# Optimization experiments

Measured on AMD Instinct MI355X. Metric: run time of the kernel, lower is better.

Reference implementation:

```python
import jax, jax.numpy as jnp
import numpy as np
import itertools

B, N, C, D = 2, 150000, 64, 128  # samples, points/sample, channels, voxel grid extent
EPS = 1e-4  # BatchNormBlock eps
# 3x3x3 submanifold kernel offsets (27 taps)
OFFS = jnp.array(list(itertools.product((-1, 0, 1), repeat=3)), dtype=jnp.int32)  # [27,3]


def setup_inputs() -> dict:
    key = jax.random.key(0)
    k1, k2 = jax.random.split(key)
    rng = np.random.default_rng(0)
    # unique voxel coordinates per sample on a D^3 grid
    pos = np.stack([
        np.stack(np.unravel_index(rng.choice(D ** 3, size=N, replace=False), (D, D, D)), axis=-1)
        for _ in range(B)
    ]).astype(np.int32)  # [B,N,3]
    feats = jax.random.normal(k1, (B, N, C), jnp.float32)
    # 4 submanifold convs (2 residual blocks x 2 convs), fan-in scaled
    Ws = jax.random.normal(k2, (4, 27, C, C), jnp.float32) / np.sqrt(27 * C)
    gammas = jnp.ones((4, C), jnp.float32)
    betas = jnp.zeros((4, C), jnp.float32)
    return {"feats": feats, "Ws": Ws, "gammas": gammas, "betas": betas, "pos": jnp.asarray(pos)}


def _build_lut(pos_b):  # pos_b: [N,3] int32 -> dense hash grid [D^3] of point index or -1
    code = (pos_b[:, 0] * D + pos_b[:, 1]) * D + pos_b[:, 2]
    return jnp.full((D ** 3,), -1, jnp.int32).at[code].set(jnp.arange(N, dtype=jnp.int32))


def _subconv(x, lut_b, pos_b, W):
    # submanifold sparse conv: per kernel tap, gather neighbor features and GEMM
    # x:[N,C], lut_b:[D^3], pos_b:[N,3], W:[27,Cin,Cout]
    def step(acc, kw):
        d, Wk = kw
        npos = pos_b + d  # [N,3]
        valid = jnp.all((npos >= 0) & (npos < D), axis=-1)
        code = (npos[:, 0] * D + npos[:, 1]) * D + npos[:, 2]
        nidx = lut_b[jnp.where(valid, code, 0)]
        valid = valid & (nidx >= 0)
        g = jnp.where(valid[:, None], x[jnp.clip(nidx, 0, N - 1)], 0.0)  # [N,Cin]
        return acc + g @ Wk, None

    acc0 = jnp.zeros((x.shape[0], W.shape[-1]), x.dtype)
    acc, _ = jax.lax.scan(step, acc0, (OFFS, W))
    return acc


def _bn_relu(x, g, b):
    # BatchNormBlock (train mode, biased var over all concatenated points) + ReLU
    mu = x.mean(axis=(0, 1))
    var = jnp.mean(jnp.square(x - mu), axis=(0, 1))
    return jax.nn.relu((x - mu) * jax.lax.rsqrt(var + EPS) * g + b)


def reference(feats, Ws, gammas, betas, pos):
    lut = jax.vmap(_build_lut)(pos)  # [B, D^3]
    conv = jax.vmap(_subconv, in_axes=(0, 0, 0, None))
    x = feats
    for blk in range(2):  # conv_block_reps ResidualBlocks (NIN is Identity since nIn==nOut)
        out1 = x
        h = _bn_relu(x, gammas[2 * blk], betas[2 * blk])
        h = conv(h, lut, pos, Ws[2 * blk])
        h = _bn_relu(h, gammas[2 * blk + 1], betas[2 * blk + 1])
        out2 = conv(h, lut, pos, Ws[2 * blk + 1])
        x = out1 + out2
    return x
```

## Files before the change

### kernel.cpp

```cpp
#include <hip/hip_runtime.h>
#include <stdint.h>

#define DGRID 128
#define D3 (DGRID * DGRID * DGRID)
#define NBATCH 2
#define NPTS 150000
#define NROWS (NBATCH * NPTS)
#define NPAD 300032
#define NWAVES (NPAD / 64)
#define NCBLK (NWAVES / 4)
#define EPSBN 1e-4f
#define SBLK 1024

typedef __attribute__((ext_vector_type(8))) short s16x8;
typedef __attribute__((ext_vector_type(4))) float f32x4;

static __device__ __forceinline__ uint32_t f2bf_rne(float f) {
  uint32_t b = __float_as_uint(f);
  return (b + 0x7FFFu + ((b >> 16) & 1u)) >> 16;
}

static __device__ __forceinline__ f32x4 mfma16(uint4 a, uint4 b, f32x4 c) {
  return __builtin_amdgcn_mfma_f32_16x16x32_bf16(
      __builtin_bit_cast(s16x8, a), __builtin_bit_cast(s16x8, b), c, 0, 0, 0);
}

__global__ void k_scatter(const int* __restrict__ pos, int* __restrict__ lut) {
  int g = blockIdx.x * blockDim.x + threadIdx.x;
  if (g >= NROWS) return;
  int b = g / NPTS;
  int i = g - b * NPTS;
  int x = pos[3 * g], y = pos[3 * g + 1], z = pos[3 * g + 2];
  lut[(size_t)b * D3 + (x * DGRID + y) * DGRID + z] = i;
}

__global__ void k_nbr(const int* __restrict__ pos, const int* __restrict__ lut,
                      int* __restrict__ nbr) {
  int g = blockIdx.x * blockDim.x + threadIdx.x;
  if (g >= NROWS) return;
  int b = g / NPTS;
  int x = pos[3 * g], y = pos[3 * g + 1], z = pos[3 * g + 2];
  const int* L = lut + (size_t)b * D3;
#pragma unroll
  for (int t = 0; t < 27; ++t) {
    int nx = x + t / 9 - 1;
    int ny = y + (t / 3) % 3 - 1;
    int nz = z + t % 3 - 1;
    int v = -1;
    if ((unsigned)nx < DGRID && (unsigned)ny < DGRID && (unsigned)nz < DGRID) {
      int n = L[(nx * DGRID + ny) * DGRID + nz];
      if (n >= 0) v = b * NPTS + n;
    }
    nbr[(size_t)t * NPAD + g] = v;
  }
}

__global__ void k_wpack(const float* __restrict__ Ws, uint4* __restrict__ Wfrag) {
  int e = blockIdx.x * 256 + threadIdx.x;
  if (e >= 4 * 27 * 512) return;
  int lane = e & 63, nb = (e >> 6) & 3, s = (e >> 8) & 1, tt = e >> 9;
  int kb = s * 32 + (lane >> 4) * 8;
  int cout = nb * 16 + (lane & 15);
  const float* src = Ws + (size_t)tt * 4096;
  uint32_t p[4];
#pragma unroll
  for (int j = 0; j < 4; ++j) {
    uint32_t lo = f2bf_rne(src[(kb + 2 * j) * 64 + cout]);
    uint32_t hi = f2bf_rne(src[(kb + 2 * j + 1) * 64 + cout]);
    p[j] = (hi << 16) | lo;
  }
  uint4 o;
  o.x = p[0]; o.y = p[1]; o.z = p[2]; o.w = p[3];
  Wfrag[e] = o;
}

__global__ void k_stats1(const float* __restrict__ X, float* __restrict__ part) {
  __shared__ float s[512];
  int c = threadIdx.x & 63, q = threadIdx.x >> 6;
  float sm = 0.f, sq = 0.f;
  for (int r = blockIdx.x * 4 + q; r < NROWS; r += SBLK * 4) {
    float v = X[(size_t)r * 64 + c];
    sm += v;
    sq += v * v;
  }
  s[threadIdx.x] = sm;
  s[256 + threadIdx.x] = sq;
  __syncthreads();
  if (q == 0) {
    sm = s[c] + s[64 + c] + s[128 + c] + s[192 + c];
    sq = s[256 + c] + s[320 + c] + s[384 + c] + s[448 + c];
    part[blockIdx.x * 128 + c] = sm;
    part[blockIdx.x * 128 + 64 + c] = sq;
  }
}

__global__ void k_stats2(const float* __restrict__ part, int nblk,
                         const float* __restrict__ gamma, const float* __restrict__ beta,
                         float* __restrict__ chanp, int cid) {
  __shared__ float s[512];
  int c = threadIdx.x & 63, q = threadIdx.x >> 6;
  float sm = 0.f, sq = 0.f;
  for (int rb = q; rb < nblk; rb += 4) {
    sm += part[rb * 128 + c];
    sq += part[rb * 128 + 64 + c];
  }
  s[threadIdx.x] = sm;
  s[256 + threadIdx.x] = sq;
  __syncthreads();
  if (q == 0) {
    sm = s[c] + s[64 + c] + s[128 + c] + s[192 + c];
    sq = s[256 + c] + s[320 + c] + s[384 + c] + s[448 + c];
    float mean = sm / (float)NROWS;
    float var = sq / (float)NROWS - mean * mean;
    float a = gamma[cid * 64 + c] * rsqrtf(var + EPSBN);
    chanp[cid * 128 + c] = a;
    chanp[cid * 128 + 64 + c] = beta[cid * 64 + c] - mean * a;
  }
}

__global__ void k_hpass(const float* __restrict__ X, const float* __restrict__ chanp,
                        int cid, uint4* __restrict__ h) {
  int g = blockIdx.x * blockDim.x + threadIdx.x;
  if (g >= NROWS * 8) return;
  int c0 = (g & 7) * 8;
  const float* cp = chanp + cid * 128;
  const float4 a0 = *(const float4*)(cp + c0);
  const float4 a1 = *(const float4*)(cp + c0 + 4);
  const float4 b0 = *(const float4*)(cp + 64 + c0);
  const float4 b1 = *(const float4*)(cp + 64 + c0 + 4);
  const float4 x0 = *(const float4*)(X + (size_t)g * 8);
  const float4 x1 = *(const float4*)(X + (size_t)g * 8 + 4);
  float v0 = fmaxf(fmaf(x0.x, a0.x, b0.x), 0.f);
  float v1 = fmaxf(fmaf(x0.y, a0.y, b0.y), 0.f);
  float v2 = fmaxf(fmaf(x0.z, a0.z, b0.z), 0.f);
  float v3 = fmaxf(fmaf(x0.w, a0.w, b0.w), 0.f);
  float v4 = fmaxf(fmaf(x1.x, a1.x, b1.x), 0.f);
  float v5 = fmaxf(fmaf(x1.y, a1.y, b1.y), 0.f);
  float v6 = fmaxf(fmaf(x1.z, a1.z, b1.z), 0.f);
  float v7 = fmaxf(fmaf(x1.w, a1.w, b1.w), 0.f);
  uint4 o;
  o.x = (f2bf_rne(v1) << 16) | f2bf_rne(v0);
  o.y = (f2bf_rne(v3) << 16) | f2bf_rne(v2);
  o.z = (f2bf_rne(v5) << 16) | f2bf_rne(v4);
  o.w = (f2bf_rne(v7) << 16) | f2bf_rne(v6);
  h[g] = o;
}

__global__ __launch_bounds__(256, 4) void k_conv(
    const uint4* __restrict__ h, const uint4* __restrict__ Wf,
    const int* __restrict__ nbr, const float* __restrict__ res,
    float* __restrict__ out, float* __restrict__ part, int do_stats) {
  __shared__ uint4 wlds[2][512];
  __shared__ float sred[2][4][4][16];
  int tid = threadIdx.x;
  int wv = tid >> 6, lane = tid & 63;
  int tbase = (blockIdx.x * 4 + wv) * 64;
  int lrow = lane & 15, lkg = lane >> 4;

  f32x4 acc[4][4];
#pragma unroll
  for (int i = 0; i < 4; i++)
#pragma unroll
    for (int j = 0; j < 4; j++) acc[i][j] = (f32x4){0.f, 0.f, 0.f, 0.f};

  wlds[0][tid] = Wf[tid];
  wlds[0][256 + tid] = Wf[256 + tid];

  int nin[4];
#pragma unroll
  for (int rt = 0; rt < 4; rt++) nin[rt] = nbr[tbase + rt * 16 + lrow];

  for (int t = 0; t < 27; t++) {
    __syncthreads();
    uint4 bf[8];
#pragma unroll
    for (int i = 0; i < 8; i++) bf[i] = wlds[t & 1][i * 64 + lane];
    uint4 nv0, nv1;
    if (t + 1 < 27) {
      nv0 = Wf[(t + 1) * 512 + tid];
      nv1 = Wf[(t + 1) * 512 + 256 + tid];
    }
    int ni[4];
#pragma unroll
    for (int rt = 0; rt < 4; rt++) ni[rt] = nin[rt];
    if (t + 1 < 27) {
#pragma unroll
      for (int rt = 0; rt < 4; rt++)
        nin[rt] = nbr[(size_t)(t + 1) * NPAD + tbase + rt * 16 + lrow];
    }
#pragma unroll
    for (int rt = 0; rt < 4; rt++) {
      uint4 a0 = {0u, 0u, 0u, 0u}, a1 = {0u, 0u, 0u, 0u};
      if (ni[rt] >= 0) {
        const uint4* hp = h + (size_t)ni[rt] * 8;
        a0 = hp[lkg];
        a1 = hp[lkg + 4];
      }
#pragma unroll
      for (int nb = 0; nb < 4; nb++) {
        acc[rt][nb] = mfma16(a0, bf[nb], acc[rt][nb]);
        acc[rt][nb] = mfma16(a1, bf[4 + nb], acc[rt][nb]);
      }
    }
    if (t + 1 < 27) {
      wlds[(t + 1) & 1][tid] = nv0;
      wlds[(t + 1) & 1][256 + tid] = nv1;
    }
  }

  float sm[4] = {0.f, 0.f, 0.f, 0.f}, sq[4] = {0.f, 0.f, 0.f, 0.f};
#pragma unroll
  for (int rt = 0; rt < 4; rt++)
#pragma unroll
    for (int r = 0; r < 4; r++) {
      int gr = tbase + rt * 16 + lkg * 4 + r;
      if (gr < NROWS) {
#pragma unroll
        for (int nb = 0; nb < 4; nb++) {
          float v = acc[rt][nb][r];
          size_t oi = (size_t)gr * 64 + nb * 16 + lrow;
          if (res) v += res[oi];
          out[oi] = v;
          sm[nb] += v;
          sq[nb] += v * v;
        }
      }
    }
  if (do_stats) {
#pragma unroll
    for (int nb = 0; nb < 4; nb++) {
      sm[nb] += __shfl_xor(sm[nb], 16, 64);
      sm[nb] += __shfl_xor(sm[nb], 32, 64);
      sq[nb] += __shfl_xor(sq[nb], 16, 64);
      sq[nb] += __shfl_xor(sq[nb], 32, 64);
    }
    if (lane < 16) {
#pragma unroll
      for (int nb = 0; nb < 4; nb++) {
        sred[0][wv][nb][lane] = sm[nb];
        sred[1][wv][nb][lane] = sq[nb];
      }
    }
    __syncthreads();
    if (tid < 64) {
      float s0 = 0.f, s1 = 0.f;
      int nb = tid >> 4, c = tid & 15;
#pragma unroll
      for (int w = 0; w < 4; w++) {
        s0 += sred[0][w][nb][c];
        s1 += sred[1][w][nb][c];
      }
      part[blockIdx.x * 128 + tid] = s0;
      part[blockIdx.x * 128 + 64 + tid] = s1;
    }
  }
}

extern "C" void kernel_launch(void* const* d_in, const int* in_sizes, int n_in,
                              void* d_out, int out_size, void* d_ws, size_t ws_size,
                              hipStream_t stream) {
  const float* feats = (const float*)d_in[0];
  const float* Ws = (const float*)d_in[1];
  const float* gammas = (const float*)d_in[2];
  const float* betas = (const float*)d_in[3];
  const int* pos = (const int*)d_in[4];
  float* out = (float*)d_out;

  char* w = (char*)d_ws;
  auto alloc = [&](size_t b) {
    char* p = w;
    w += (b + 255) & ~(size_t)255;
    return p;
  };
  int* nbr = (int*)alloc((size_t)27 * NPAD * 4);
  uint4* Wfrag = (uint4*)alloc((size_t)4 * 27 * 512 * 16);
  float* part = (float*)alloc((size_t)NCBLK * 128 * 4);
  float* chanp = (float*)alloc((size_t)4 * 128 * 4);
  uint4* h = (uint4*)alloc((size_t)NPAD * 128);
  float* xbuf = (float*)alloc((size_t)NROWS * 64 * 4);
  char* reg0 = alloc((size_t)NROWS * 64 * 4);
  float* cbuf = (float*)reg0;
  int* lut = (int*)reg0;

  hipMemsetAsync(lut, 0xFF, (size_t)NBATCH * D3 * 4, stream);
  hipMemsetAsync(nbr, 0xFF, (size_t)27 * NPAD * 4, stream);
  int gpts = (NROWS + 255) / 256;
  k_scatter<<<gpts, 256, 0, stream>>>(pos, lut);
  k_nbr<<<gpts, 256, 0, stream>>>(pos, lut, nbr);
  k_wpack<<<216, 256, 0, stream>>>(Ws, Wfrag);

  k_stats1<<<SBLK, 256, 0, stream>>>(feats, part);
  k_stats2<<<1, 256, 0, stream>>>(part, SBLK, gammas, betas, chanp, 0);
  k_hpass<<<9375, 256, 0, stream>>>(feats, chanp, 0, h);
  k_conv<<<NCBLK, 256, 0, stream>>>(h, Wfrag + 0 * 27 * 512, nbr, nullptr, cbuf, part, 1);

  k_stats2<<<1, 256, 0, stream>>>(part, NCBLK, gammas, betas, chanp, 1);
  k_hpass<<<9375, 256, 0, stream>>>(cbuf, chanp, 1, h);
  k_conv<<<NCBLK, 256, 0, stream>>>(h, Wfrag + 1 * 27 * 512, nbr, feats, xbuf, part, 1);

  k_stats2<<<1, 256, 0, stream>>>(part, NCBLK, gammas, betas, chanp, 2);
  k_hpass<<<9375, 256, 0, stream>>>(xbuf, chanp, 2, h);
  k_conv<<<NCBLK, 256, 0, stream>>>(h, Wfrag + 2 * 27 * 512, nbr, nullptr, cbuf, part, 1);

  k_stats2<<<1, 256, 0, stream>>>(part, NCBLK, gammas, betas, chanp, 3);
  k_hpass<<<9375, 256, 0, stream>>>(cbuf, chanp, 3, h);
  k_conv<<<NCBLK, 256, 0, stream>>>(h, Wfrag + 3 * 27 * 512, nbr, xbuf, out, part, 0);
}
```

Baseline: 1.478 ms.

## Pipeline neighbor gathers across taps with zero-row sentinel and coalesced LDS epilogue

Missing neighbors now point at a dedicated zero row appended to h, so the gather becomes branchless. The conv loop is software-pipelined two taps at a time: the next tap's neighbor features are prefetched while MFMAs run on the current one. Weights are read straight from global/L2 instead of a double-buffered LDS copy, which drops the per-tap barrier. The epilogue transposes accumulators through an LDS slab so outputs and residuals move as coalesced float4, at the cost of more registers, per-row-tile barriers and removal of the occupancy hint.

```diff
diff --git a/kernel.cpp b/kernel.cpp
--- a/kernel.cpp
+++ b/kernel.cpp
@@ -7,8 +7,8 @@
 #define NPTS 150000
 #define NROWS (NBATCH * NPTS)
 #define NPAD 300032
-#define NWAVES (NPAD / 64)
-#define NCBLK (NWAVES / 4)
+#define ZROW NROWS
+#define NCBLK (NPAD / 256)
 #define EPSBN 1e-4f
 #define SBLK 1024
 
@@ -37,7 +37,12 @@
 __global__ void k_nbr(const int* __restrict__ pos, const int* __restrict__ lut,
                       int* __restrict__ nbr) {
   int g = blockIdx.x * blockDim.x + threadIdx.x;
-  if (g >= NROWS) return;
+  if (g >= NPAD) return;
+  if (g >= NROWS) {
+#pragma unroll
+    for (int t = 0; t < 27; ++t) nbr[(size_t)t * NPAD + g] = ZROW;
+    return;
+  }
   int b = g / NPTS;
   int x = pos[3 * g], y = pos[3 * g + 1], z = pos[3 * g + 2];
   const int* L = lut + (size_t)b * D3;
@@ -46,7 +51,7 @@
     int nx = x + t / 9 - 1;
     int ny = y + (t / 3) % 3 - 1;
     int nz = z + t % 3 - 1;
-    int v = -1;
+    int v = ZROW;
     if ((unsigned)nx < DGRID && (unsigned)ny < DGRID && (unsigned)nz < DGRID) {
       int n = L[(nx * DGRID + ny) * DGRID + nz];
       if (n >= 0) v = b * NPTS + n;
@@ -121,7 +126,11 @@
 __global__ void k_hpass(const float* __restrict__ X, const float* __restrict__ chanp,
                         int cid, uint4* __restrict__ h) {
   int g = blockIdx.x * blockDim.x + threadIdx.x;
-  if (g >= NROWS * 8) return;
+  if (g >= (NROWS + 1) * 8) return;
+  if (g >= NROWS * 8) {
+    h[g] = (uint4){0u, 0u, 0u, 0u};
+    return;
+  }
   int c0 = (g & 7) * 8;
   const float* cp = chanp + cid * 128;
   const float4 a0 = *(const float4*)(cp + c0);
@@ -146,14 +155,23 @@
   h[g] = o;
 }
 
-__global__ __launch_bounds__(256, 4) void k_conv(
+#define MFMA_HALF(AREG, WOFF)                                            \
+  {                                                                      \
+    uint4 wf[4];                                                         \
+    _Pragma("unroll") for (int nb = 0; nb < 4; nb++) wf[nb] =            \
+        Wt[(WOFF) + nb * 64];                                            \
+    _Pragma("unroll") for (int rt = 0; rt < 4; rt++)                     \
+        _Pragma("unroll") for (int nb = 0; nb < 4; nb++) acc[rt][nb] =   \
+            mfma16(AREG, wf[nb], acc[rt][nb]);                           \
+  }
+
+__global__ __launch_bounds__(256) void k_conv(
     const uint4* __restrict__ h, const uint4* __restrict__ Wf,
     const int* __restrict__ nbr, const float* __restrict__ res,
     float* __restrict__ out, float* __restrict__ part, int do_stats) {
-  __shared__ uint4 wlds[2][512];
+  __shared__ float xp[4][16 * 68];
   __shared__ float sred[2][4][4][16];
-  int tid = threadIdx.x;
-  int wv = tid >> 6, lane = tid & 63;
+  int tid = threadIdx.x, wv = tid >> 6, lane = tid & 63;
   int tbase = (blockIdx.x * 4 + wv) * 64;
   int lrow = lane & 15, lkg = lane >> 4;
 
@@ -163,92 +181,109 @@
 #pragma unroll
     for (int j = 0; j < 4; j++) acc[i][j] = (f32x4){0.f, 0.f, 0.f, 0.f};
 
-  wlds[0][tid] = Wf[tid];
-  wlds[0][256 + tid] = Wf[256 + tid];
-
-  int nin[4];
-#pragma unroll
-  for (int rt = 0; rt < 4; rt++) nin[rt] = nbr[tbase + rt * 16 + lrow];
-
-  for (int t = 0; t < 27; t++) {
+  const int* nb0 = nbr + tbase + lrow;
+  int niA[4], niB[4];
+  uint4 aA[4][2], aB[4][2];
+#pragma unroll
+  for (int rt = 0; rt < 4; rt++) niA[rt] = nb0[rt * 16];
+#pragma unroll
+  for (int rt = 0; rt < 4; rt++) {
+    const uint4* hp = h + (size_t)niA[rt] * 8 + lkg;
+    aA[rt][0] = hp[0];
+    aA[rt][1] = hp[4];
+  }
+#pragma unroll
+  for (int rt = 0; rt < 4; rt++) niB[rt] = nb0[(size_t)NPAD + rt * 16];
+
+  for (int t = 0; t < 26; t += 2) {
+#pragma unroll
+    for (int rt = 0; rt < 4; rt++) niA[rt] = nb0[(size_t)(t + 2) * NPAD + rt * 16];
+#pragma unroll
+    for (int rt = 0; rt < 4; rt++) {
+      const uint4* hp = h + (size_t)niB[rt] * 8 + lkg;
+      aB[rt][0] = hp[0];
+      aB[rt][1] = hp[4];
+    }
+    {
+      const uint4* Wt = Wf + (size_t)t * 512 + lane;
+      MFMA_HALF(aA[rt][0], 0)
+      MFMA_HALF(aA[rt][1], 256)
+    }
+    int t3 = (t + 3 < 27) ? t + 3 : 26;
+#pragma unroll
+    for (int rt = 0; rt < 4; rt++) niB[rt] = nb0[(size_t)t3 * NPAD + rt * 16];
+#pragma unroll
+    for (int rt = 0; rt < 4; rt++) {
+      const uint4* hp = h + (size_t)niA[rt] * 8 + lkg;
+      aA[rt][0] = hp[0];
+      aA[rt][1] = hp[4];
+    }
+    {
+      const uint4* Wt = Wf + (size_t)(t + 1) * 512 + lane;
+      MFMA_HALF(aB[rt][0], 0)
+      MFMA_HALF(aB[rt][1], 256)
+    }
+  }
+  {
+    const uint4* Wt = Wf + (size_t)26 * 512 + lane;
+    MFMA_HALF(aA[rt][0], 0)
+    MFMA_HALF(aA[rt][1], 256)
+  }
+
+  float smc[16], sqc[16];
+#pragma unroll
+  for (int j = 0; j < 16; j++) smc[j] = sqc[j] = 0.f;
+  float* slab = xp[wv];
+#pragma unroll 1
+  for (int rt = 0; rt < 4; rt++) {
+#pragma unroll
+    for (int nb = 0; nb < 4; nb++)
+#pragma unroll
+      for (int r = 0; r < 4; r++)
+        slab[(lkg * 4 + r) * 68 + nb * 16 + lrow] = acc[rt][nb][r];
     __syncthreads();
-    uint4 bf[8];
-#pragma unroll
-    for (int i = 0; i < 8; i++) bf[i] = wlds[t & 1][i * 64 + lane];
-    uint4 nv0, nv1;
-    if (t + 1 < 27) {
-      nv0 = Wf[(t + 1) * 512 + tid];
-      nv1 = Wf[(t + 1) * 512 + 256 + tid];
-    }
-    int ni[4];
-#pragma unroll
-    for (int rt = 0; rt < 4; rt++) ni[rt] = nin[rt];
-    if (t + 1 < 27) {
-#pragma unroll
-      for (int rt = 0; rt < 4; rt++)
-        nin[rt] = nbr[(size_t)(t + 1) * NPAD + tbase + rt * 16 + lrow];
-    }
-#pragma unroll
-    for (int rt = 0; rt < 4; rt++) {
-      uint4 a0 = {0u, 0u, 0u, 0u}, a1 = {0u, 0u, 0u, 0u};
-      if (ni[rt] >= 0) {
-        const uint4* hp = h + (size_t)ni[rt] * 8;
-        a0 = hp[lkg];
-        a1 = hp[lkg + 4];
+    int gr = tbase + rt * 16 + lrow;
+    if (gr < NROWS) {
+#pragma unroll
+      for (int j = 0; j < 4; j++) {
+        float4 vv = *(float4*)&slab[lrow * 68 + lkg * 16 + j * 4];
+        size_t off = (size_t)gr * 64 + lkg * 16 + j * 4;
+        if (res) {
+          float4 rr = *(const float4*)(res + off);
+          vv.x += rr.x; vv.y += rr.y; vv.z += rr.z; vv.w += rr.w;
+        }
+        *(float4*)(out + off) = vv;
+        smc[j * 4 + 0] += vv.x; sqc[j * 4 + 0] += vv.x * vv.x;
+        smc[j * 4 + 1] += vv.y; sqc[j * 4 + 1] += vv.y * vv.y;
+        smc[j * 4 + 2] += vv.z; sqc[j * 4 + 2] += vv.z * vv.z;
+        smc[j * 4 + 3] += vv.w; sqc[j * 4 + 3] += vv.w * vv.w;
       }
-#pragma unroll
-      for (int nb = 0; nb < 4; nb++) {
-        acc[rt][nb] = mfma16(a0, bf[nb], acc[rt][nb]);
-        acc[rt][nb] = mfma16(a1, bf[4 + nb], acc[rt][nb]);
-      }
-    }
-    if (t + 1 < 27) {
-      wlds[(t + 1) & 1][tid] = nv0;
-      wlds[(t + 1) & 1][256 + tid] = nv1;
-    }
-  }
-
-  float sm[4] = {0.f, 0.f, 0.f, 0.f}, sq[4] = {0.f, 0.f, 0.f, 0.f};
-#pragma unroll
-  for (int rt = 0; rt < 4; rt++)
-#pragma unroll
-    for (int r = 0; r < 4; r++) {
-      int gr = tbase + rt * 16 + lkg * 4 + r;
-      if (gr < NROWS) {
-#pragma unroll
-        for (int nb = 0; nb < 4; nb++) {
-          float v = acc[rt][nb][r];
-          size_t oi = (size_t)gr * 64 + nb * 16 + lrow;
-          if (res) v += res[oi];
-          out[oi] = v;
-          sm[nb] += v;
-          sq[nb] += v * v;
-        }
-      }
-    }
+    }
+    __syncthreads();
+  }
   if (do_stats) {
 #pragma unroll
-    for (int nb = 0; nb < 4; nb++) {
-      sm[nb] += __shfl_xor(sm[nb], 16, 64);
-      sm[nb] += __shfl_xor(sm[nb], 32, 64);
-      sq[nb] += __shfl_xor(sq[nb], 16, 64);
-      sq[nb] += __shfl_xor(sq[nb], 32, 64);
-    }
-    if (lane < 16) {
-#pragma unroll
-      for (int nb = 0; nb < 4; nb++) {
-        sred[0][wv][nb][lane] = sm[nb];
-        sred[1][wv][nb][lane] = sq[nb];
+    for (int j = 0; j < 16; j++) {
+      smc[j] += __shfl_xor(smc[j], 1); sqc[j] += __shfl_xor(sqc[j], 1);
+      smc[j] += __shfl_xor(smc[j], 2); sqc[j] += __shfl_xor(sqc[j], 2);
+      smc[j] += __shfl_xor(smc[j], 4); sqc[j] += __shfl_xor(sqc[j], 4);
+      smc[j] += __shfl_xor(smc[j], 8); sqc[j] += __shfl_xor(sqc[j], 8);
+    }
+    if (lrow == 0) {
+#pragma unroll
+      for (int j = 0; j < 16; j++) {
+        sred[0][wv][lkg][j] = smc[j];
+        sred[1][wv][lkg][j] = sqc[j];
       }
     }
     __syncthreads();
     if (tid < 64) {
       float s0 = 0.f, s1 = 0.f;
-      int nb = tid >> 4, c = tid & 15;
+      int q = tid >> 4, c = tid & 15;
 #pragma unroll
       for (int w = 0; w < 4; w++) {
-        s0 += sred[0][w][nb][c];
-        s1 += sred[1][w][nb][c];
+        s0 += sred[0][w][q][c];
+        s1 += sred[1][w][q][c];
       }
       part[blockIdx.x * 128 + tid] = s0;
       part[blockIdx.x * 128 + 64 + tid] = s1;
@@ -283,26 +318,25 @@
   int* lut = (int*)reg0;
 
   hipMemsetAsync(lut, 0xFF, (size_t)NBATCH * D3 * 4, stream);
-  hipMemsetAsync(nbr, 0xFF, (size_t)27 * NPAD * 4, stream);
   int gpts = (NROWS + 255) / 256;
   k_scatter<<<gpts, 256, 0, stream>>>(pos, lut);
-  k_nbr<<<gpts, 256, 0, stream>>>(pos, lut, nbr);
+  k_nbr<<<NPAD / 256, 256, 0, stream>>>(pos, lut, nbr);
   k_wpack<<<216, 256, 0, stream>>>(Ws, Wfrag);
 
   k_stats1<<<SBLK, 256, 0, stream>>>(feats, part);
   k_stats2<<<1, 256, 0, stream>>>(part, SBLK, gammas, betas, chanp, 0);
-  k_hpass<<<9375, 256, 0, stream>>>(feats, chanp, 0, h);
+  k_hpass<<<9376, 256, 0, stream>>>(feats, chanp, 0, h);
   k_conv<<<NCBLK, 256, 0, stream>>>(h, Wfrag + 0 * 27 * 512, nbr, nullptr, cbuf, part, 1);
 
   k_stats2<<<1, 256, 0, stream>>>(part, NCBLK, gammas, betas, chanp, 1);
-  k_hpass<<<9375, 256, 0, stream>>>(cbuf, chanp, 1, h);
+  k_hpass<<<9376, 256, 0, stream>>>(cbuf, chanp, 1, h);
   k_conv<<<NCBLK, 256, 0, stream>>>(h, Wfrag + 1 * 27 * 512, nbr, feats, xbuf, part, 1);
 
   k_stats2<<<1, 256, 0, stream>>>(part, NCBLK, gammas, betas, chanp, 2);
-  k_hpass<<<9375, 256, 0, stream>>>(xbuf, chanp, 2, h);
+  k_hpass<<<9376, 256, 0, stream>>>(xbuf, chanp, 2, h);
   k_conv<<<NCBLK, 256, 0, stream>>>(h, Wfrag + 2 * 27 * 512, nbr, nullptr, cbuf, part, 1);
 
   k_stats2<<<1, 256, 0, stream>>>(part, NCBLK, gammas, betas, chanp, 3);
-  k_hpass<<<9375, 256, 0, stream>>>(cbuf, chanp, 3, h);
+  k_hpass<<<9376, 256, 0, stream>>>(cbuf, chanp, 3, h);
   k_conv<<<NCBLK, 256, 0, stream>>>(h, Wfrag + 3 * 27 * 512, nbr, xbuf, out, part, 0);
 }
```

After: 1.188 ms. 19.6% less time.
